# Performance work log

Measured on AMD Instinct MI355X. Metric: run time of the kernel, lower is better.

Reference implementation:

```python
import jax, jax.numpy as jnp
import numpy as np

EPS = 1e-5
RATES = (1, 6, 12, 18)


def _bn(x, g, b, m, v):
    # eval-mode BatchNorm2d: x [B,C,H,W], params [C]
    inv = g / jnp.sqrt(v + EPS)
    return x * inv[None, :, None, None] + (b - m * inv)[None, :, None, None]


def setup_inputs() -> dict:
    key = jax.random.key(0)
    ks = jax.random.split(key, 20)
    B, C, H, W = 8, 512, 96, 96
    Cq = C // 4  # 128 channels per branch, depthwise (groups=128)
    f32 = jnp.float32
    inp = {}
    inp["x"] = jax.random.normal(ks[0], (B, C, H, W), f32)
    # four depthwise 3x3 conv branches (stacked over branch axis)
    inp["wdw"] = jax.random.normal(ks[1], (4, Cq, 1, 3, 3), f32) * 0.1
    inp["bdw"] = jax.random.normal(ks[2], (4, Cq), f32) * 0.01
    inp["gdw"] = jnp.ones((4, Cq), f32) + 0.1 * jax.random.normal(ks[3], (4, Cq), f32)
    inp["bedw"] = jax.random.normal(ks[4], (4, Cq), f32) * 0.01
    inp["mdw"] = jax.random.normal(ks[5], (4, Cq), f32) * 0.01
    inp["vdw"] = jax.random.uniform(ks[6], (4, Cq), f32, 0.5, 1.5)
    # out_s: shared 1x1 conv 4->4 + bn(4)
    inp["ws"] = jax.random.normal(ks[7], (4, 4, 1, 1), f32) * 0.5
    inp["bs"] = jax.random.normal(ks[8], (4,), f32) * 0.01
    inp["gs"] = jnp.ones((4,), f32) + 0.1 * jax.random.normal(ks[9], (4,), f32)
    inp["bes"] = jax.random.normal(ks[10], (4,), f32) * 0.01
    inp["ms"] = jax.random.normal(ks[11], (4,), f32) * 0.01
    inp["vs"] = jax.random.uniform(ks[12], (4,), f32, 0.5, 1.5)
    # out: 1x1 conv 512->512 + bn(512)
    inp["wo"] = jax.random.normal(ks[13], (C, C, 1, 1), f32) * (1.0 / np.sqrt(C))
    inp["bo"] = jax.random.normal(ks[14], (C,), f32) * 0.01
    inp["go"] = jnp.ones((C,), f32) + 0.1 * jax.random.normal(ks[15], (C,), f32)
    inp["beo"] = jax.random.normal(ks[16], (C,), f32) * 0.01
    inp["mo"] = jax.random.normal(ks[17], (C,), f32) * 0.01
    inp["vo"] = jax.random.uniform(ks[18], (C,), f32, 0.5, 1.5)
    return inp


def reference(x, wdw, bdw, gdw, bedw, mdw, vdw, ws, bs, gs, bes, ms, vs,
              wo, bo, go, beo, mo, vo):
    B = x.shape[0]
    Cq = wdw.shape[1]  # 128
    xs = jnp.split(x, 4, axis=1)  # four [B,Cq,H,W] chunks
    branches = []
    for i, r in enumerate(RATES):
        y = jax.lax.conv_general_dilated(
            xs[i], wdw[i], window_strides=(1, 1),
            padding=[(r, r), (r, r)], rhs_dilation=(r, r),
            dimension_numbers=("NCHW", "OIHW", "NCHW"),
            feature_group_count=Cq)
        y = y + bdw[i][None, :, None, None]
        y = jax.nn.relu(_bn(y, gdw[i], bedw[i], mdw[i], vdw[i]))
        branches.append(y)
    # Per-channel loop in the original == shared 1x1 conv over the branch axis.
    z = jnp.stack(branches, axis=2)  # [B, Cq, 4, H, W]
    W4 = ws[:, :, 0, 0]  # [4,4]
    z = jnp.einsum("oi,bcihw->bcohw", W4, z) + bs[None, None, :, None, None]
    inv_s = gs / jnp.sqrt(vs + EPS)
    z = jax.nn.relu(z * inv_s[None, None, :, None, None]
                    + (bes - ms * inv_s)[None, None, :, None, None])
    # concat order: channel c contributes its 4 out_s channels consecutively
    z = z.reshape(B, Cq * 4, z.shape[3], z.shape[4])  # [B,512,H,W]
    # final 1x1 conv 512->512 + bn + relu
    Wo = wo[:, :, 0, 0]
    out = jnp.einsum("oi,bihw->bohw", Wo, z) + bo[None, :, None, None]
    out = jax.nn.relu(_bn(out, go, beo, mo, vo))
    return out
```

## Files before the change

### kernel.cpp

```cpp
#include <hip/hip_runtime.h>
#include <cstdint>
#include <cstddef>

typedef float  f32x4 __attribute__((ext_vector_type(4)));
typedef float  f32x2 __attribute__((ext_vector_type(2)));
typedef short  s16x8 __attribute__((ext_vector_type(8)));
typedef short  s16x4 __attribute__((ext_vector_type(4)));
typedef unsigned int u32x4 __attribute__((ext_vector_type(4)));

#define EPSV 1e-5f

__device__ __forceinline__ float rfl(float v) {
  return __builtin_bit_cast(float, __builtin_amdgcn_readfirstlane(__builtin_bit_cast(int, v)));
}
__device__ __forceinline__ unsigned pk2(float a, float b) {
  unsigned short ua = __builtin_bit_cast(unsigned short, (__bf16)a);
  unsigned short ub = __builtin_bit_cast(unsigned short, (__bf16)b);
  return (unsigned)ua | ((unsigned)ub << 16);
}
__device__ __forceinline__ void gll16(const void* g, void* l) {
  __builtin_amdgcn_global_load_lds((const __attribute__((address_space(1))) unsigned int*)g,
                                   (__attribute__((address_space(3))) unsigned int*)l, 16, 0, 0);
}
__device__ __forceinline__ f32x4 relu4(f32x4 v) {
  f32x4 r; r.x = fmaxf(v.x,0.f); r.y = fmaxf(v.y,0.f); r.z = fmaxf(v.z,0.f); r.w = fmaxf(v.w,0.f);
  return r;
}

__global__ void kF(const float* __restrict__ wo, const float* __restrict__ bo,
                   const float* __restrict__ go, const float* __restrict__ beo,
                   const float* __restrict__ mo, const float* __restrict__ vo,
                   __bf16* __restrict__ wopp, float* __restrict__ co)
{
  const int oc = blockIdx.x;
  const int k  = threadIdx.x;
  float invo = go[oc] * rsqrtf(vo[oc] + EPSV);
  float v = wo[(size_t)oc*512 + k] * invo;
  int mt = oc >> 7, ocl = oc & 127;
  int kt = k >> 6, kk = (k >> 5) & 1, g = (k >> 3) & 3, jj = k & 7;
  size_t dst = (size_t)(mt*8 + kt)*10240 + (size_t)kk*5120 + ocl*40 + g*8 + jj;
  wopp[dst] = (__bf16)v;
  if (k == 0) co[oc] = bo[oc]*invo + beo[oc] - mo[oc]*invo;
}

__global__ __launch_bounds__(768, 6) void kA(const float* __restrict__ x,
    const float* __restrict__ wdw, const float* __restrict__ bdw, const float* __restrict__ gdw,
    const float* __restrict__ bedw, const float* __restrict__ mdw, const float* __restrict__ vdw,
    const float* __restrict__ w4, const float* __restrict__ bsc, const float* __restrict__ gsc,
    const float* __restrict__ besc, const float* __restrict__ msc, const float* __restrict__ vsc,
    __bf16* __restrict__ z2s)
{
  __shared__ alignas(16) float sp[96*136];
  const int tid = threadIdx.x;
  const int b = blockIdx.x >> 7, c = blockIdx.x & 127;

  float wf[4][9], cdwv[4], w4f[4][4], c4v[4];
  #pragma unroll
  for (int i = 0; i < 4; ++i) {
    int idx = i*128 + c;
    float inv = gdw[idx] * rsqrtf(vdw[idx] + EPSV);
    #pragma unroll
    for (int t = 0; t < 9; ++t) wf[i][t] = rfl(wdw[(size_t)idx*9 + t] * inv);
    cdwv[i] = rfl(bdw[idx]*inv + bedw[idx] - mdw[idx]*inv);
  }
  #pragma unroll
  for (int o = 0; o < 4; ++o) {
    float invs = gsc[o] * rsqrtf(vsc[o] + EPSV);
    #pragma unroll
    for (int i = 0; i < 4; ++i) w4f[o][i] = rfl(w4[o*4 + i] * invs);
    c4v[o] = rfl(bsc[o]*invs + besc[o] - msc[o]*invs);
  }

  for (int z = tid; z < 96*40; z += 768) {
    int row = z / 40, cw = z - row*40;
    sp[row*136 + (cw < 20 ? cw : 96 + cw)] = 0.f;
  }

  const int wq = tid % 24;
  const int hb = (tid / 24) * 3;
  const int w0 = wq * 4;

  const f32x4* xv = (const f32x4*)x;
  const size_t gbase = (size_t)(b*512 + c) * 2304;

  int srow[3], scol[3];
  #pragma unroll
  for (int k = 0; k < 3; ++k) { int g = tid + k*768; srow[k] = g/24; scol[k] = g - srow[k]*24; }

  f32x4 zacc[4][3];
  #pragma unroll
  for (int o = 0; o < 4; ++o)
    #pragma unroll
    for (int k = 0; k < 3; ++k)
      zacc[o][k] = (f32x4){c4v[o], c4v[o], c4v[o], c4v[o]};

  const int RR[4] = {1, 6, 12, 18};

  #pragma unroll
  for (int i = 0; i < 4; ++i) {
    __syncthreads();
    #pragma unroll
    for (int k = 0; k < 3; ++k) {
      f32x4 v = xv[gbase + (size_t)i*294912 + (size_t)(tid + k*768)];
      *(f32x4*)(sp + srow[k]*136 + 20 + scol[k]*4) = v;
    }
    __syncthreads();

    const int r = RR[i];
    #pragma unroll
    for (int k = 0; k < 3; ++k) {
      const int h = hb + k;
      f32x4 acc = {0.f, 0.f, 0.f, 0.f};
      #pragma unroll
      for (int dh = -1; dh <= 1; ++dh) {
        const int h2 = h + dh*r;
        if ((unsigned)h2 < 96u) {
          const float* row = sp + h2*136 + 20 + w0;
          f32x4 tc = *(const f32x4*)row;
          f32x4 tl, tr;
          if (i == 0) {
            f32x2 a  = *(const f32x2*)(row - 2);
            f32x2 bb = *(const f32x2*)(row + 4);
            tl = (f32x4){a.y, tc.x, tc.y, tc.z};
            tr = (f32x4){tc.y, tc.z, tc.w, bb.x};
          } else if (r == 12) {
            tl = *(const f32x4*)(row - 12);
            tr = *(const f32x4*)(row + 12);
          } else {
            f32x2 a0 = *(const f32x2*)(row - r), a1 = *(const f32x2*)(row - r + 2);
            f32x2 b0 = *(const f32x2*)(row + r), b1 = *(const f32x2*)(row + r + 2);
            tl = (f32x4){a0.x, a0.y, a1.x, a1.y};
            tr = (f32x4){b0.x, b0.y, b1.x, b1.y};
          }
          const int wb = (dh + 1) * 3;
          acc += wf[i][wb]*tl + wf[i][wb+1]*tc + wf[i][wb+2]*tr;
        }
      }
      f32x4 y = relu4(acc + cdwv[i]);
      #pragma unroll
      for (int o = 0; o < 4; ++o) zacc[o][k] += w4f[o][i]*y;
    }
  }

  __bf16* zbase = z2s + (size_t)(b*128 + c) * 36864;
  #pragma unroll
  for (int k = 0; k < 3; ++k) {
    const int h = hb + k;
    f32x4 z[4];
    #pragma unroll
    for (int o = 0; o < 4; ++o) z[o] = relu4(zacc[o][k]);
    u32x4 s0 = { pk2(z[0].x,z[1].x), pk2(z[2].x,z[3].x), pk2(z[0].y,z[1].y), pk2(z[2].y,z[3].y) };
    u32x4 s1 = { pk2(z[0].z,z[1].z), pk2(z[2].z,z[3].z), pk2(z[0].w,z[1].w), pk2(z[2].w,z[3].w) };
    u32x4* dst = (u32x4*)(zbase + (size_t)(h*24 + wq)*16);
    dst[0] = s0;
    dst[1] = s1;
  }
}

__global__ __launch_bounds__(256) void kB(const void* __restrict__ wopp_,
    const void* __restrict__ z2s_, const float* __restrict__ co, float* __restrict__ out)
{
  __shared__ alignas(16) char lA[20480];
  __shared__ alignas(16) char lB[16384];
  const char* wopp = (const char*)wopp_;
  const char* z2s  = (const char*)z2s_;

  const int tid = threadIdx.x;
  const int lane = tid & 63, wv = tid >> 6;
  const int wm = wv >> 1, wn = wv & 1;
  const int pt = blockIdx.x;
  const int mt = blockIdx.y;
  const int b  = blockIdx.z;
  const int pix0 = pt * 128;
  const int l15 = lane & 15, lg = lane >> 4;

  f32x4 acc[4][4] = {};

  for (int kt = 0; kt < 8; ++kt) {
    const char* srcA = wopp + (size_t)(mt*8 + kt)*20480;
    for (int j = wv; j < 20; j += 4)
      gll16(srcA + j*1024 + lane*16, lA + j*1024);
    #pragma unroll
    for (int ct4 = 0; ct4 < 4; ++ct4) {
      int ct = wv*4 + ct4;
      const char* srcB = z2s + ((size_t)(b*128 + kt*16 + ct)*36864 + (size_t)pix0*4)*2;
      gll16(srcB + lane*16, lB + ct*1024);
    }
    __syncthreads();

    #pragma unroll
    for (int kk = 0; kk < 2; ++kk) {
      s16x8 af[4];
      #pragma unroll
      for (int m = 0; m < 4; ++m)
        af[m] = *(const s16x8*)(lA + kk*10240 + (wm*64 + m*16 + l15)*80 + lg*16);
      #pragma unroll
      for (int n = 0; n < 4; ++n) {
        const char* p = lB + kk*8192 + lg*2048 + (wn*64 + n*16 + l15)*8;
        s16x4 lo = *(const s16x4*)(p);
        s16x4 hi = *(const s16x4*)(p + 1024);
        s16x8 bfr = __builtin_shufflevector(lo, hi, 0,1,2,3,4,5,6,7);
        #pragma unroll
        for (int m = 0; m < 4; ++m)
          acc[m][n] = __builtin_amdgcn_mfma_f32_16x16x32_bf16(af[m], bfr, acc[m][n], 0, 0, 0);
      }
    }
    __syncthreads();
  }

  const int colp = pix0 + wn*64 + l15;
  #pragma unroll
  for (int m = 0; m < 4; ++m) {
    const int ocb = mt*128 + wm*64 + m*16 + lg*4;
    #pragma unroll
    for (int r2 = 0; r2 < 4; ++r2) {
      const int oc = ocb + r2;
      const float cov = co[oc];
      float* orow = out + ((size_t)(b*512 + oc))*9216 + colp;
      #pragma unroll
      for (int n = 0; n < 4; ++n) {
        float v = acc[m][n][r2] + cov;
        orow[(size_t)n*16] = fmaxf(v, 0.f);
      }
    }
  }
}

extern "C" void kernel_launch(void* const* d_in, const int* in_sizes, int n_in,
                              void* d_out, int out_size, void* d_ws, size_t ws_size,
                              hipStream_t stream)
{
  (void)in_sizes; (void)out_size;
  if (n_in < 19) return;
  const size_t Z2_BYTES = 75497472;
  const size_t WOPP_BYTES = 655360;
  if (ws_size < Z2_BYTES + WOPP_BYTES + 2048) return;

  const float* x    = (const float*)d_in[0];
  const float* wdw  = (const float*)d_in[1];
  const float* bdw  = (const float*)d_in[2];
  const float* gdw  = (const float*)d_in[3];
  const float* bedw = (const float*)d_in[4];
  const float* mdw  = (const float*)d_in[5];
  const float* vdw  = (const float*)d_in[6];
  const float* w4   = (const float*)d_in[7];
  const float* bs   = (const float*)d_in[8];
  const float* gs   = (const float*)d_in[9];
  const float* bes  = (const float*)d_in[10];
  const float* ms   = (const float*)d_in[11];
  const float* vs   = (const float*)d_in[12];
  const float* wo   = (const float*)d_in[13];
  const float* bo   = (const float*)d_in[14];
  const float* go   = (const float*)d_in[15];
  const float* beo  = (const float*)d_in[16];
  const float* mo   = (const float*)d_in[17];
  const float* vo   = (const float*)d_in[18];

  __bf16* z2s  = (__bf16*)d_ws;
  __bf16* wopp = (__bf16*)((char*)d_ws + Z2_BYTES);
  float*  co   = (float*)((char*)d_ws + Z2_BYTES + WOPP_BYTES);

  kF<<<512, 512, 0, stream>>>(wo, bo, go, beo, mo, vo, wopp, co);
  kA<<<1024, 768, 0, stream>>>(x, wdw, bdw, gdw, bedw, mdw, vdw, w4, bs, gs, bes, ms, vs, z2s);
  kB<<<dim3(72, 4, 8), 256, 0, stream>>>(wopp, z2s, co, (float*)d_out);
}
```

Measured before the change: 124.8 us.

## Split depthwise kernel into half-image tiles with 8-wide per-thread strips

The depthwise/branch-mix kernel now launches two blocks per (batch, channel), each covering 48 output rows and staging 66 rows (including an 18-row halo) into a smaller LDS buffer. Each thread computes one row of 8 contiguous pixels instead of three rows of 4, which reuses loaded neighbours within registers and writes 64 contiguous bytes of output. This aims to raise parallelism and occupancy and cut LDS reads per output. The cost is redundant halo loads from global memory, about 37% extra input traffic.

```diff
diff --git a/kernel.cpp b/kernel.cpp
--- a/kernel.cpp
+++ b/kernel.cpp
@@ -21,10 +21,6 @@
 __device__ __forceinline__ void gll16(const void* g, void* l) {
   __builtin_amdgcn_global_load_lds((const __attribute__((address_space(1))) unsigned int*)g,
                                    (__attribute__((address_space(3))) unsigned int*)l, 16, 0, 0);
-}
-__device__ __forceinline__ f32x4 relu4(f32x4 v) {
-  f32x4 r; r.x = fmaxf(v.x,0.f); r.y = fmaxf(v.y,0.f); r.z = fmaxf(v.z,0.f); r.w = fmaxf(v.w,0.f);
-  return r;
 }
 
 __global__ void kF(const float* __restrict__ wo, const float* __restrict__ bo,
@@ -43,16 +39,22 @@
   if (k == 0) co[oc] = bo[oc]*invo + beo[oc] - mo[oc]*invo;
 }
 
-__global__ __launch_bounds__(768, 6) void kA(const float* __restrict__ x,
+__global__ __launch_bounds__(576, 7) void kA(const float* __restrict__ x,
     const float* __restrict__ wdw, const float* __restrict__ bdw, const float* __restrict__ gdw,
     const float* __restrict__ bedw, const float* __restrict__ mdw, const float* __restrict__ vdw,
     const float* __restrict__ w4, const float* __restrict__ bsc, const float* __restrict__ gsc,
     const float* __restrict__ besc, const float* __restrict__ msc, const float* __restrict__ vsc,
     __bf16* __restrict__ z2s)
 {
-  __shared__ alignas(16) float sp[96*136];
+  __shared__ alignas(16) float sp[84*136];
   const int tid = threadIdx.x;
-  const int b = blockIdx.x >> 7, c = blockIdx.x & 127;
+  const int bc = blockIdx.x >> 1;
+  const int half = blockIdx.x & 1;
+  const int b = bc >> 7, c = bc & 127;
+  const int h0 = half * 48;
+  const int loc0 = h0 - 18;
+  const int gstart = half ? 30 : 0;
+  const int Lbase  = half ? 0 : 18;
 
   float wf[4][9], cdwv[4], w4f[4][4], c4v[4];
   #pragma unroll
@@ -71,90 +73,104 @@
     c4v[o] = rfl(bsc[o]*invs + besc[o] - msc[o]*invs);
   }
 
-  for (int z = tid; z < 96*40; z += 768) {
+  for (int z = tid; z < 84*40; z += 576) {
     int row = z / 40, cw = z - row*40;
     sp[row*136 + (cw < 20 ? cw : 96 + cw)] = 0.f;
   }
 
-  const int wq = tid % 24;
-  const int hb = (tid / 24) * 3;
-  const int w0 = wq * 4;
+  const int colg = tid % 12;
+  const int rowt = tid / 12;
+  const int h  = h0 + rowt;
+  const int w0 = colg * 8;
 
   const f32x4* xv = (const f32x4*)x;
   const size_t gbase = (size_t)(b*512 + c) * 2304;
 
-  int srow[3], scol[3];
-  #pragma unroll
-  for (int k = 0; k < 3; ++k) { int g = tid + k*768; srow[k] = g/24; scol[k] = g - srow[k]*24; }
-
-  f32x4 zacc[4][3];
+  float zacc[4][8];
   #pragma unroll
   for (int o = 0; o < 4; ++o)
     #pragma unroll
-    for (int k = 0; k < 3; ++k)
-      zacc[o][k] = (f32x4){c4v[o], c4v[o], c4v[o], c4v[o]};
-
-  const int RR[4] = {1, 6, 12, 18};
+    for (int j = 0; j < 8; ++j) zacc[o][j] = c4v[o];
 
   #pragma unroll
   for (int i = 0; i < 4; ++i) {
     __syncthreads();
-    #pragma unroll
-    for (int k = 0; k < 3; ++k) {
-      f32x4 v = xv[gbase + (size_t)i*294912 + (size_t)(tid + k*768)];
-      *(f32x4*)(sp + srow[k]*136 + 20 + scol[k]*4) = v;
-    }
-    __syncthreads();
-
-    const int r = RR[i];
-    #pragma unroll
-    for (int k = 0; k < 3; ++k) {
-      const int h = hb + k;
-      f32x4 acc = {0.f, 0.f, 0.f, 0.f};
-      #pragma unroll
-      for (int dh = -1; dh <= 1; ++dh) {
-        const int h2 = h + dh*r;
-        if ((unsigned)h2 < 96u) {
-          const float* row = sp + h2*136 + 20 + w0;
-          f32x4 tc = *(const f32x4*)row;
-          f32x4 tl, tr;
-          if (i == 0) {
-            f32x2 a  = *(const f32x2*)(row - 2);
-            f32x2 bb = *(const f32x2*)(row + 4);
-            tl = (f32x4){a.y, tc.x, tc.y, tc.z};
-            tr = (f32x4){tc.y, tc.z, tc.w, bb.x};
-          } else if (r == 12) {
-            tl = *(const f32x4*)(row - 12);
-            tr = *(const f32x4*)(row + 12);
-          } else {
-            f32x2 a0 = *(const f32x2*)(row - r), a1 = *(const f32x2*)(row - r + 2);
-            f32x2 b0 = *(const f32x2*)(row + r), b1 = *(const f32x2*)(row + r + 2);
-            tl = (f32x4){a0.x, a0.y, a1.x, a1.y};
-            tr = (f32x4){b0.x, b0.y, b1.x, b1.y};
-          }
-          const int wb = (dh + 1) * 3;
-          acc += wf[i][wb]*tl + wf[i][wb+1]*tc + wf[i][wb+2]*tr;
+    for (int idx = tid; idx < 1584; idx += 576) {
+      int rr = idx / 24, cc = idx - rr*24;
+      f32x4 v = xv[gbase + (size_t)i*294912 + (size_t)(gstart + rr)*24 + cc];
+      *(f32x4*)(sp + (Lbase + rr)*136 + 20 + cc*4) = v;
+    }
+    __syncthreads();
+
+    const int r = (i == 0) ? 1 : (i == 1) ? 6 : (i == 2) ? 12 : 18;
+    float acc[8];
+    #pragma unroll
+    for (int j = 0; j < 8; ++j) acc[j] = 0.f;
+
+    #pragma unroll
+    for (int dh = -1; dh <= 1; ++dh) {
+      const int h2 = h + dh*r;
+      if ((unsigned)h2 < 96u) {
+        const float* row = sp + (h2 - loc0)*136 + 20 + w0;
+        const float wl = wf[i][(dh+1)*3], wc = wf[i][(dh+1)*3+1], wr = wf[i][(dh+1)*3+2];
+        if (i == 0) {
+          float s[12];
+          #pragma unroll
+          for (int t = 0; t < 6; ++t) *(f32x2*)(s + 2*t) = *(const f32x2*)(row - 2 + 2*t);
+          #pragma unroll
+          for (int j = 0; j < 8; ++j)
+            acc[j] += wl*s[j+1] + wc*s[j+2] + wr*s[j+3];
+        } else if (i == 1) {
+          float s[20];
+          #pragma unroll
+          for (int t = 0; t < 10; ++t) *(f32x2*)(s + 2*t) = *(const f32x2*)(row - 6 + 2*t);
+          #pragma unroll
+          for (int j = 0; j < 8; ++j)
+            acc[j] += wl*s[j] + wc*s[j+6] + wr*s[j+12];
+        } else if (i == 2) {
+          float tl[8], tc[8], tr[8];
+          *(f32x4*)(tl)   = *(const f32x4*)(row - 12); *(f32x4*)(tl+4) = *(const f32x4*)(row - 8);
+          *(f32x4*)(tc)   = *(const f32x4*)(row);      *(f32x4*)(tc+4) = *(const f32x4*)(row + 4);
+          *(f32x4*)(tr)   = *(const f32x4*)(row + 12); *(f32x4*)(tr+4) = *(const f32x4*)(row + 16);
+          #pragma unroll
+          for (int j = 0; j < 8; ++j)
+            acc[j] += wl*tl[j] + wc*tc[j] + wr*tr[j];
+        } else {
+          float tl[8], tc[8], tr[8];
+          #pragma unroll
+          for (int t = 0; t < 4; ++t) *(f32x2*)(tl + 2*t) = *(const f32x2*)(row - 18 + 2*t);
+          *(f32x4*)(tc)   = *(const f32x4*)(row);      *(f32x4*)(tc+4) = *(const f32x4*)(row + 4);
+          #pragma unroll
+          for (int t = 0; t < 4; ++t) *(f32x2*)(tr + 2*t) = *(const f32x2*)(row + 18 + 2*t);
+          #pragma unroll
+          for (int j = 0; j < 8; ++j)
+            acc[j] += wl*tl[j] + wc*tc[j] + wr*tr[j];
         }
       }
-      f32x4 y = relu4(acc + cdwv[i]);
-      #pragma unroll
-      for (int o = 0; o < 4; ++o) zacc[o][k] += w4f[o][i]*y;
-    }
-  }
-
-  __bf16* zbase = z2s + (size_t)(b*128 + c) * 36864;
-  #pragma unroll
-  for (int k = 0; k < 3; ++k) {
-    const int h = hb + k;
-    f32x4 z[4];
-    #pragma unroll
-    for (int o = 0; o < 4; ++o) z[o] = relu4(zacc[o][k]);
-    u32x4 s0 = { pk2(z[0].x,z[1].x), pk2(z[2].x,z[3].x), pk2(z[0].y,z[1].y), pk2(z[2].y,z[3].y) };
-    u32x4 s1 = { pk2(z[0].z,z[1].z), pk2(z[2].z,z[3].z), pk2(z[0].w,z[1].w), pk2(z[2].w,z[3].w) };
-    u32x4* dst = (u32x4*)(zbase + (size_t)(h*24 + wq)*16);
-    dst[0] = s0;
-    dst[1] = s1;
-  }
+    }
+    #pragma unroll
+    for (int j = 0; j < 8; ++j) {
+      float y = fmaxf(acc[j] + cdwv[i], 0.f);
+      #pragma unroll
+      for (int o = 0; o < 4; ++o) zacc[o][j] += w4f[o][i]*y;
+    }
+  }
+
+  float z0[8], z1[8], z2[8], z3[8];
+  #pragma unroll
+  for (int j = 0; j < 8; ++j) {
+    z0[j] = fmaxf(zacc[0][j], 0.f);
+    z1[j] = fmaxf(zacc[1][j], 0.f);
+    z2[j] = fmaxf(zacc[2][j], 0.f);
+    z3[j] = fmaxf(zacc[3][j], 0.f);
+  }
+  __bf16* zb = z2s + (size_t)(b*128 + c)*36864 + (size_t)(h*24 + colg*2)*16;
+  u32x4* dst = (u32x4*)zb;
+  u32x4 s0 = { pk2(z0[0],z1[0]), pk2(z2[0],z3[0]), pk2(z0[1],z1[1]), pk2(z2[1],z3[1]) };
+  u32x4 s1 = { pk2(z0[2],z1[2]), pk2(z2[2],z3[2]), pk2(z0[3],z1[3]), pk2(z2[3],z3[3]) };
+  u32x4 s2 = { pk2(z0[4],z1[4]), pk2(z2[4],z3[4]), pk2(z0[5],z1[5]), pk2(z2[5],z3[5]) };
+  u32x4 s3 = { pk2(z0[6],z1[6]), pk2(z2[6],z3[6]), pk2(z0[7],z1[7]), pk2(z2[7],z3[7]) };
+  dst[0] = s0; dst[1] = s1; dst[2] = s2; dst[3] = s3;
 }
 
 __global__ __launch_bounds__(256) void kB(const void* __restrict__ wopp_,
@@ -261,6 +277,6 @@
   float*  co   = (float*)((char*)d_ws + Z2_BYTES + WOPP_BYTES);
 
   kF<<<512, 512, 0, stream>>>(wo, bo, go, beo, mo, vo, wopp, co);
-  kA<<<1024, 768, 0, stream>>>(x, wdw, bdw, gdw, bedw, mdw, vdw, w4, bs, gs, bes, ms, vs, z2s);
+  kA<<<2048, 576, 0, stream>>>(x, wdw, bdw, gdw, bedw, mdw, vdw, w4, bs, gs, bes, ms, vs, z2s);
   kB<<<dim3(72, 4, 8), 256, 0, stream>>>(wopp, z2s, co, (float*)d_out);
 }
```

New measurement: 170.7 us. 36.8% more time.
